# Kernel tuning notes

Hardware: AMD Instinct MI355X
Metric: run time of the kernel (lower is better)

The kernel has to match this reference:

```python
import jax, jax.numpy as jnp
import numpy as np

N, R, A, F, T, O = 50000, 5, 8, 128, 2, 128
RADIUS = 1.0

def _template_vertices():
    # polar grid of template vertices in cartesian coords, shape (R, A, 2)
    radii = (np.arange(1, R + 1) / R) * RADIUS
    angles = np.linspace(0.0, 2.0 * np.pi, A, endpoint=False)
    x = radii[:, None] * np.cos(angles)[None, :]
    y = radii[:, None] * np.sin(angles)[None, :]
    return np.stack([x, y], axis=-1)

def _interp_coeffs():
    # Gaussian interpolation coefficients (concrete define_interpolation_coefficients),
    # shape (R, A, R*A), rows normalized -- constant, non-trainable (built in build()).
    v = _template_vertices().reshape(R * A, 2)
    d2 = ((v[:, None, :] - v[None, :, :]) ** 2).sum(-1)
    sigma = RADIUS / R
    w = np.exp(-d2 / (2.0 * sigma ** 2))
    w = w / w.sum(axis=1, keepdims=True)
    return w.reshape(R, A, R * A).astype(np.float32)

def setup_inputs() -> dict:
    key = jax.random.key(0)
    k1, k2, k3, k4, k5 = jax.random.split(key, 5)
    mesh_signal = jax.random.normal(k1, (N, F), dtype=jnp.float32)
    bary_w = jax.random.uniform(k2, (N, R, A, 3), dtype=jnp.float32)
    bary_w = bary_w / bary_w.sum(axis=-1, keepdims=True)  # barycentric weights sum to 1
    bary_idx = jax.random.randint(k3, (N, R, A, 3), 0, N, dtype=jnp.int32)
    glorot = lambda k, shp: jax.random.uniform(
        k, shp, jnp.float32, -1.0, 1.0) * np.sqrt(6.0 / (shp[-1] + shp[-2]))
    template_weights = glorot(k4, (A, T, O, F))  # (n_angular, templates, out, feat)
    bias = glorot(k5, (T, O))
    return {"mesh_signal": mesh_signal, "bary_w": bary_w,
            "template_weights": template_weights, "bias": bias,
            "interp_coeffs": jnp.asarray(_interp_coeffs()),
            "bary_idx": bary_idx}

def reference(mesh_signal, bary_w, template_weights, bias, interp_coeffs, bary_idx):
    # --- patch operator: barycentric gather + interpolation ---
    gathered = mesh_signal[bary_idx]                       # (N,R,A,3,F) irregular gather
    interp = (bary_w[..., None] * gathered).sum(axis=-2)   # (N,R,A,F)
    # prior: mix all R*A template-vertex signals per output template vertex
    sig = interp.reshape(-1, R * A, F)                     # (N,RA,F)
    interp = jnp.einsum('nkf,rak->nraf', sig, interp_coeffs)  # (N,R,A,F)
    # --- fold: all A rotations (rotation_delta=1), vectorized by rolling weights ---
    rots = jnp.arange(0, A, 1)                             # K = A rotations
    idx = (jnp.arange(A)[None, :] + rots[:, None]) % A     # (K,A): roll(interp,+r) == roll(W,-r)
    W_all = template_weights[idx]                          # (K,A,T,O,F)
    # TF adds bias before summing over (R,A) axes -> bias appears R*A times
    z = jnp.einsum('nraf,katof->nkto', interp, W_all) + (R * A) * bias  # (N,K,T,O)
    out = jax.nn.relu(z).sum(axis=2)                       # sum over templates -> (N,K,O)
    return out
```

## Files before the change

### kernel.cpp

```cpp
#include <hip/hip_runtime.h>
#include <hip/hip_bf16.h>
#include <stdint.h>

#define NN 50000
#define RR 5
#define AA 8
#define FF 128
#define TT 2
#define OO 128
#define KDIM 1024
#define KB 512
#define RA 40

typedef __attribute__((ext_vector_type(8))) short short8;
typedef __attribute__((ext_vector_type(4))) float f32x4;
typedef __attribute__((ext_vector_type(4))) int i32x4;

__device__ inline void gload_lds16(const void* g, void* l) {
  __builtin_amdgcn_global_load_lds(
      (const __attribute__((address_space(1))) unsigned int*)g,
      (__attribute__((address_space(3))) unsigned int*)l, 16, 0, 0);
}

__global__ void prep_kernel(const float* __restrict__ mesh,
                            const float* __restrict__ coeffs,
                            const float* __restrict__ W,
                            const float* __restrict__ bary_w,
                            const int* __restrict__ bary_idx,
                            __hip_bfloat16* __restrict__ meshq,
                            float* __restrict__ G,
                            __hip_bfloat16* __restrict__ Bh,
                            unsigned* __restrict__ packb,
                            int do_pack) {
  int tid = blockIdx.x * blockDim.x + threadIdx.x;
  int stride = gridDim.x * blockDim.x;
  for (int i = tid; i < NN * FF; i += stride) {
    int n = i >> 7, f = i & 127;
    int p = f >> 5, fo = f & 31;
    meshq[((long)p * NN + n) * 32 + fo] = __float2bfloat16(mesh[i]);
  }
  for (int i = tid; i < AA * RA; i += stride) {
    int p = i / RA, k = i % RA;
    int a = p & 3;
    float s1 = 0.f, s2 = 0.f;
    for (int r = 0; r < RR; ++r) {
      s1 += coeffs[(r * AA + a) * RA + k];
      s2 += coeffs[(r * AA + a + 4) * RA + k];
    }
    G[i] = (p < 4) ? (s1 + s2) : (s1 - s2);
  }
  for (int i = tid; i < 2048 * KB; i += stride) {
    int col = i >> 9, k = i & 511;
    int half = col >> 10, c = col & 1023;
    int o = c >> 3, t = (c >> 2) & 1, j = c & 3;
    int a4 = k >> 7, f = k & 127;
    int m = (a4 + j) & 3;
    float w0 = W[((m * TT + t) * OO + o) * FF + f];
    float w4 = W[(((m + 4) * TT + t) * OO + o) * FF + f];
    float v;
    if (half == 0) v = 0.5f * (w0 + w4);
    else {
      v = 0.5f * (w0 - w4);
      if (a4 + j >= 4) v = -v;
    }
    Bh[i] = __float2bfloat16(v);
  }
  if (do_pack) {
    for (int i = tid; i < NN * 120; i += stride) {
      __hip_bfloat16 h = __float2bfloat16(bary_w[i]);
      unsigned wb = *(unsigned short*)&h;
      packb[i] = ((unsigned)bary_idx[i] << 16) | wb;
    }
  }
}

__global__ __launch_bounds__(256) void s_pass_packed(
    const __hip_bfloat16* __restrict__ meshq,
    const unsigned* __restrict__ packb,
    const float* __restrict__ G,
    __hip_bfloat16* __restrict__ Sout,
    int p) {
  __shared__ unsigned pk_s[16 * 120];
  __shared__ float g_s[AA * RA];
  int tid = threadIdx.x;
  long n0 = (long)blockIdx.x * 16;
  const i32x4* psrc = (const i32x4*)(packb + n0 * 120);
  for (int i = tid; i < 480; i += 256) {
    i32x4 v = __builtin_nontemporal_load(psrc + i);
    ((i32x4*)pk_s)[i] = v;
  }
  for (int i = tid; i < AA * RA; i += 256) g_s[i] = G[i];
  __syncthreads();

  int g = tid >> 4;
  int fo = tid & 15;
  long n = n0 + g;
  const unsigned* pg = pk_s + g * 120;
  const char* mbase = (const char*)meshq + (long)p * NN * 64 + fo * 4;

  float sx_acc[AA], sy_acc[AA];
#pragma unroll
  for (int a = 0; a < AA; ++a) { sx_acc[a] = 0.f; sy_acc[a] = 0.f; }

#pragma unroll 2
  for (int k = 0; k < RA; ++k) {
    float sx = 0.f, sy = 0.f;
#pragma unroll
    for (int j = 0; j < 3; ++j) {
      unsigned v = pg[k * 3 + j];
      unsigned row = v >> 16;
      float w = __uint_as_float(v << 16);
      unsigned u = *(const unsigned*)(mbase + (long)row * 64);
      sx += w * __uint_as_float(u << 16);
      sy += w * __uint_as_float(u & 0xffff0000u);
    }
#pragma unroll
    for (int a = 0; a < AA; ++a) {
      float c = g_s[a * RA + k];
      sx_acc[a] += c * sx;
      sy_acc[a] += c * sy;
    }
  }

  long base = n * KDIM + p * 32 + fo * 2;
#pragma unroll
  for (int a = 0; a < AA; ++a) {
    __hip_bfloat16 hx = __float2bfloat16(sx_acc[a]);
    __hip_bfloat16 hy = __float2bfloat16(sy_acc[a]);
    unsigned u = (unsigned)*(unsigned short*)&hx | ((unsigned)*(unsigned short*)&hy << 16);
    __builtin_nontemporal_store(u, (unsigned*)(Sout + base + a * FF));
  }
}

__global__ __launch_bounds__(256) void s_pass_kernel(
    const __hip_bfloat16* __restrict__ meshq,
    const float* __restrict__ bary_w,
    const int* __restrict__ bary_idx,
    const float* __restrict__ G,
    __hip_bfloat16* __restrict__ Sout,
    int p) {
  __shared__ float w_s[16 * 120];
  __shared__ int i_s[16 * 120];
  __shared__ float g_s[AA * RA];
  int tid = threadIdx.x;
  long n0 = (long)blockIdx.x * 16;
  const f32x4* wsrc = (const f32x4*)(bary_w + n0 * 120);
  const i32x4* isrc = (const i32x4*)(bary_idx + n0 * 120);
  for (int i = tid; i < 480; i += 256) {
    f32x4 wv = __builtin_nontemporal_load(wsrc + i);
    ((f32x4*)w_s)[i] = wv;
    i32x4 iv = __builtin_nontemporal_load(isrc + i);
    ((i32x4*)i_s)[i] = iv;
  }
  for (int i = tid; i < AA * RA; i += 256) g_s[i] = G[i];
  __syncthreads();
  int g = tid >> 4;
  int fo = tid & 15;
  long n = n0 + g;
  const float* wg = w_s + g * 120;
  const int* ig = i_s + g * 120;
  const char* mbase = (const char*)meshq + (long)p * NN * 64 + fo * 4;
  float sx_acc[AA], sy_acc[AA];
#pragma unroll
  for (int a = 0; a < AA; ++a) { sx_acc[a] = 0.f; sy_acc[a] = 0.f; }
#pragma unroll 2
  for (int k = 0; k < RA; ++k) {
    float sx = 0.f, sy = 0.f;
#pragma unroll
    for (int j = 0; j < 3; ++j) {
      int row = ig[k * 3 + j];
      unsigned u = *(const unsigned*)(mbase + (long)row * 64);
      float w = wg[k * 3 + j];
      sx += w * __uint_as_float(u << 16);
      sy += w * __uint_as_float(u & 0xffff0000u);
    }
#pragma unroll
    for (int a = 0; a < AA; ++a) {
      float c = g_s[a * RA + k];
      sx_acc[a] += c * sx;
      sy_acc[a] += c * sy;
    }
  }
  long base = n * KDIM + p * 32 + fo * 2;
#pragma unroll
  for (int a = 0; a < AA; ++a) {
    __hip_bfloat16 hx = __float2bfloat16(sx_acc[a]);
    __hip_bfloat16 hy = __float2bfloat16(sy_acc[a]);
    unsigned u = (unsigned)*(unsigned short*)&hx | ((unsigned)*(unsigned short*)&hy << 16);
    __builtin_nontemporal_store(u, (unsigned*)(Sout + base + a * FF));
  }
}

__global__ __launch_bounds__(256, 2) void gemm_kernel(
    const __hip_bfloat16* __restrict__ Sh,
    const __hip_bfloat16* __restrict__ Bh,
    const float* __restrict__ bias,
    float* __restrict__ out) {
  int bx = blockIdx.x;
  int by = blockIdx.y;
  int cb = by & 7;
  int mt = ((by >> 3) << 3) + bx;
  if (mt >= 391) return;
  int row0 = mt * 128;
  int cE0 = cb * 128;

  int tid = threadIdx.x;
  int lane = tid & 63;
  int wid = tid >> 6;
  int wave_m = wid >> 1;
  int wave_n = wid & 1;

  __shared__ __align__(16) char lds[79872];

  long srcSp[2], srcB[2];
  int dstA[2], dstBd[2];
#pragma unroll
  for (int i = 0; i < 2; ++i) {
    int li = i * 256 + tid;
    int r = li >> 2, sp = li & 3;
    int sl = sp ^ ((r >> 1) & 3);
    int rowA = row0 + r;
    if (rowA >= NN) rowA = NN - 1;
    srcSp[i] = (long)rowA * KDIM + sl * 8;
    dstA[i] = li * 16;
    srcB[i] = (long)(cE0 + r) * KB + sl * 8;
    dstBd[i] = 16384 + li * 16;
  }
  int offA[4], offB[4];
#pragma unroll
  for (int m = 0; m < 4; ++m) {
    int r = wave_m * 64 + m * 16 + (lane & 15);
    int phys = (lane >> 4) ^ ((r >> 1) & 3);
    offA[m] = r * 64 + phys * 16;
  }
#pragma unroll
  for (int n = 0; n < 4; ++n) {
    int c = wave_n * 64 + n * 16 + (lane & 15);
    int phys = (lane >> 4) ^ ((c >> 1) & 3);
    offB[n] = 16384 + c * 64 + phys * 16;
  }

  f32x4 acc[4][8];
#pragma unroll
  for (int m = 0; m < 4; ++m)
#pragma unroll
    for (int q = 0; q < 8; ++q) acc[m][q] = (f32x4){0.f, 0.f, 0.f, 0.f};

#define STAGE(T)                                                              \
  {                                                                           \
    char* base_ = lds + ((T) & 1) * 32768;                                    \
    long k0_ = (long)(T) * 32;                                                \
    _Pragma("unroll") for (int i_ = 0; i_ < 2; ++i_)                          \
        gload_lds16(Sh + srcSp[i_] + k0_, base_ + dstA[i_]);                  \
    _Pragma("unroll") for (int i_ = 0; i_ < 2; ++i_)                          \
        gload_lds16(Sh + srcSp[i_] + 512 + k0_, base_ + 8192 + dstA[i_]);     \
    _Pragma("unroll") for (int i_ = 0; i_ < 2; ++i_)                          \
        gload_lds16(Bh + srcB[i_] + k0_, base_ + dstBd[i_]);                  \
    _Pragma("unroll") for (int i_ = 0; i_ < 2; ++i_)                          \
        gload_lds16(Bh + srcB[i_] + (long)1024 * KB + k0_,                    \
                    base_ + 8192 + dstBd[i_]);                                \
  }

#define GSTEP(STP, DOSTAGE)                                                   \
  {                                                                           \
    const char* cbuf = lds + ((STP) & 1) * 32768;                             \
    asm volatile("s_waitcnt vmcnt(0)" ::: "memory");                          \
    __builtin_amdgcn_sched_barrier(0);                                        \
    __builtin_amdgcn_s_barrier();                                             \
    __builtin_amdgcn_sched_barrier(0);                                        \
    short8 aE[4], aO[4], bE[4], bO[4];                                        \
    _Pragma("unroll") for (int m_ = 0; m_ < 4; ++m_) {                        \
      aE[m_] = *(const short8*)(cbuf + offA[m_]);                             \
      aO[m_] = *(const short8*)(cbuf + offA[m_] + 8192);                      \
    }                                                                         \
    _Pragma("unroll") for (int n_ = 0; n_ < 4; ++n_) {                        \
      bE[n_] = *(const short8*)(cbuf + offB[n_]);                             \
      bO[n_] = *(const short8*)(cbuf + offB[n_] + 8192);                      \
    }                                                                         \
    if (DOSTAGE) STAGE((STP) + 1)                                             \
    __builtin_amdgcn_s_setprio(1);                                            \
    _Pragma("unroll") for (int m_ = 0; m_ < 4; ++m_)                          \
        _Pragma("unroll") for (int n_ = 0; n_ < 4; ++n_) {                    \
      acc[m_][n_] = __builtin_amdgcn_mfma_f32_16x16x32_bf16(                  \
          aE[m_], bE[n_], acc[m_][n_], 0, 0, 0);                              \
      acc[m_][n_ + 4] = __builtin_amdgcn_mfma_f32_16x16x32_bf16(              \
          aO[m_], bO[n_], acc[m_][n_ + 4], 0, 0, 0);                          \
    }                                                                         \
    __builtin_amdgcn_s_setprio(0);                                            \
    __builtin_amdgcn_sched_barrier(0);                                        \
  }

  STAGE(0)
  GSTEP(0, 1)  GSTEP(1, 1)  GSTEP(2, 1)  GSTEP(3, 1)
  GSTEP(4, 1)  GSTEP(5, 1)  GSTEP(6, 1)  GSTEP(7, 1)
  GSTEP(8, 1)  GSTEP(9, 1)  GSTEP(10, 1) GSTEP(11, 1)
  GSTEP(12, 1) GSTEP(13, 1) GSTEP(14, 1) GSTEP(15, 0)

  __syncthreads();
  float* lout = (float*)lds;
  int c = lane & 15;
  int t = (c >> 2) & 1;
  int j = c & 3;
  int hi = lane >> 4;
  float bq[4];
#pragma unroll
  for (int n = 0; n < 4; ++n) {
    int o_l = wave_n * 8 + n * 2 + (c >> 3);
    bq[n] = 40.f * bias[t * OO + cb * 16 + o_l];
  }
#pragma unroll
  for (int m = 0; m < 4; ++m) {
#pragma unroll
    for (int n = 0; n < 4; ++n) {
      int o_l = wave_n * 8 + n * 2 + (c >> 3);
#pragma unroll
      for (int i = 0; i < 4; ++i) {
        float zE = acc[m][n][i];
        float zO = acc[m][n + 4][i];
        float rlo = fmaxf(zE + zO + bq[n], 0.f);
        float rhi = fmaxf(zE - zO + bq[n], 0.f);
        rlo += __shfl_xor(rlo, 4);
        rhi += __shfl_xor(rhi, 4);
        if (!(lane & 4)) {
          int node = wave_m * 64 + m * 16 + hi * 4 + i;
          lout[node * 156 + j * 20 + o_l] = rlo;
          lout[node * 156 + (j + 4) * 20 + o_l] = rhi;
        }
      }
    }
  }
  __syncthreads();

#pragma unroll
  for (int it = 0; it < 16; ++it) {
    int gi = it * 256 + tid;
    int node = gi >> 5;
    int rem = gi & 31;
    int kr = rem >> 2, o4 = rem & 3;
    int grow = row0 + node;
    if (grow < NN) {
      f32x4 v = *(const f32x4*)(lout + node * 156 + kr * 20 + o4 * 4);
      long gaddr = (long)grow * 1024 + kr * 128 + cb * 16 + o4 * 4;
      __builtin_nontemporal_store(v, (f32x4*)(out + gaddr));
    }
  }
}

extern "C" void kernel_launch(void* const* d_in, const int* in_sizes, int n_in,
                              void* d_out, int out_size, void* d_ws, size_t ws_size,
                              hipStream_t stream) {
  const float* mesh   = (const float*)d_in[0];
  const float* bary_w = (const float*)d_in[1];
  const float* W      = (const float*)d_in[2];
  const float* bias   = (const float*)d_in[3];
  const float* coeffs = (const float*)d_in[4];
  const int* bidx     = (const int*)d_in[5];
  float* out = (float*)d_out;
  char* ws = (char*)d_ws;

  __hip_bfloat16* meshq = (__hip_bfloat16*)ws;
  float* G              = (float*)(ws + 12800000);
  __hip_bfloat16* Bh    = (__hip_bfloat16*)(ws + 12801280);
  __hip_bfloat16* Smat  = (__hip_bfloat16*)(ws + 16995584);
  unsigned* packb       = (unsigned*)(ws + 119395584);

  int do_pack = (ws_size >= 143395584UL) ? 1 : 0;

  prep_kernel<<<dim3(2048), dim3(256), 0, stream>>>(mesh, coeffs, W, bary_w, bidx,
                                                    meshq, G, Bh, packb, do_pack);
  if (do_pack) {
    for (int p = 0; p < 4; ++p)
      s_pass_packed<<<dim3(3125), dim3(256), 0, stream>>>(meshq, packb, G, Smat, p);
  } else {
    for (int p = 0; p < 4; ++p)
      s_pass_kernel<<<dim3(3125), dim3(256), 0, stream>>>(meshq, bary_w, bidx, G, Smat, p);
  }
  gemm_kernel<<<dim3(8, 392), dim3(256), 0, stream>>>(Smat, Bh, bias, out);
}
```

Before: 388.8 us.

## Widen gather per thread with packed FMA and issue GEMM prefetch earlier

The packed gather pass now handles 32 nodes per block with 8 threads per node. Each thread loads 8 bytes (4 bf16 features) per neighbor and accumulates them with packed f32x2 FMAs, halving the block count and doubling work per thread. This is meant to cut gather instruction count and per-block packb staging overhead, at the cost of fewer threads in flight to hide the random gather latency. Separately, the GEMM main loop now issues the next-stage global-to-LDS copies right after the barrier, before the LDS fragment reads, to start the memory traffic sooner.

New measurement: 375.6 us. 1.04x faster.

```diff
diff --git a/kernel.cpp b/kernel.cpp
--- a/kernel.cpp
+++ b/kernel.cpp
@@ -14,7 +14,21 @@
 
 typedef __attribute__((ext_vector_type(8))) short short8;
 typedef __attribute__((ext_vector_type(4))) float f32x4;
+typedef __attribute__((ext_vector_type(2))) float f32x2;
 typedef __attribute__((ext_vector_type(4))) int i32x4;
+typedef __attribute__((ext_vector_type(2))) unsigned u32x2;
+
+#if __has_builtin(__builtin_elementwise_fma)
+__device__ inline f32x2 pk_fma(f32x2 a, f32x2 b, f32x2 c) {
+  return __builtin_elementwise_fma(a, b, c);
+}
+#else
+__device__ inline f32x2 pk_fma(f32x2 a, f32x2 b, f32x2 c) {
+  f32x2 d;
+  asm("v_pk_fma_f32 %0, %1, %2, %3" : "=v"(d) : "v"(a), "v"(b), "v"(c));
+  return d;
+}
+#endif
 
 __device__ inline void gload_lds16(const void* g, void* l) {
   __builtin_amdgcn_global_load_lds(
@@ -80,55 +94,73 @@
     const float* __restrict__ G,
     __hip_bfloat16* __restrict__ Sout,
     int p) {
-  __shared__ unsigned pk_s[16 * 120];
+  __shared__ unsigned pk_s[32 * 120];
   __shared__ float g_s[AA * RA];
   int tid = threadIdx.x;
-  long n0 = (long)blockIdx.x * 16;
+  long n0 = (long)blockIdx.x * 32;
+  int nnode = (NN - n0 < 32) ? (int)(NN - n0) : 32;
+  int nvec = nnode * 30;
   const i32x4* psrc = (const i32x4*)(packb + n0 * 120);
-  for (int i = tid; i < 480; i += 256) {
+  for (int i = tid; i < nvec; i += 256) {
     i32x4 v = __builtin_nontemporal_load(psrc + i);
     ((i32x4*)pk_s)[i] = v;
   }
   for (int i = tid; i < AA * RA; i += 256) g_s[i] = G[i];
   __syncthreads();
 
-  int g = tid >> 4;
-  int fo = tid & 15;
+  int g = tid >> 3;
+  int fo = tid & 7;
   long n = n0 + g;
+  if (n >= NN) return;
   const unsigned* pg = pk_s + g * 120;
-  const char* mbase = (const char*)meshq + (long)p * NN * 64 + fo * 4;
-
-  float sx_acc[AA], sy_acc[AA];
-#pragma unroll
-  for (int a = 0; a < AA; ++a) { sx_acc[a] = 0.f; sy_acc[a] = 0.f; }
+  const char* mbase = (const char*)meshq + (long)p * NN * 64 + fo * 8;
+
+  f32x2 accA[AA], accB[AA];
+#pragma unroll
+  for (int a = 0; a < AA; ++a) {
+    accA[a] = (f32x2){0.f, 0.f};
+    accB[a] = (f32x2){0.f, 0.f};
+  }
 
 #pragma unroll 2
   for (int k = 0; k < RA; ++k) {
-    float sx = 0.f, sy = 0.f;
+    f32x2 sA = (f32x2){0.f, 0.f}, sB = (f32x2){0.f, 0.f};
 #pragma unroll
     for (int j = 0; j < 3; ++j) {
       unsigned v = pg[k * 3 + j];
-      unsigned row = v >> 16;
+      long row = v >> 16;
       float w = __uint_as_float(v << 16);
-      unsigned u = *(const unsigned*)(mbase + (long)row * 64);
-      sx += w * __uint_as_float(u << 16);
-      sy += w * __uint_as_float(u & 0xffff0000u);
+      f32x2 wv = (f32x2){w, w};
+      u32x2 u = *(const u32x2*)(mbase + row * 64);
+      f32x2 lo = (f32x2){__uint_as_float(u[0] << 16),
+                         __uint_as_float(u[0] & 0xffff0000u)};
+      f32x2 hi = (f32x2){__uint_as_float(u[1] << 16),
+                         __uint_as_float(u[1] & 0xffff0000u)};
+      sA = pk_fma(wv, lo, sA);
+      sB = pk_fma(wv, hi, sB);
     }
 #pragma unroll
     for (int a = 0; a < AA; ++a) {
-      float c = g_s[a * RA + k];
-      sx_acc[a] += c * sx;
-      sy_acc[a] += c * sy;
-    }
-  }
-
-  long base = n * KDIM + p * 32 + fo * 2;
+      float cc = g_s[a * RA + k];
+      f32x2 cv = (f32x2){cc, cc};
+      accA[a] = pk_fma(cv, sA, accA[a]);
+      accB[a] = pk_fma(cv, sB, accB[a]);
+    }
+  }
+
+  long base = n * KDIM + p * 32 + fo * 4;
 #pragma unroll
   for (int a = 0; a < AA; ++a) {
-    __hip_bfloat16 hx = __float2bfloat16(sx_acc[a]);
-    __hip_bfloat16 hy = __float2bfloat16(sy_acc[a]);
-    unsigned u = (unsigned)*(unsigned short*)&hx | ((unsigned)*(unsigned short*)&hy << 16);
-    __builtin_nontemporal_store(u, (unsigned*)(Sout + base + a * FF));
+    __hip_bfloat16 h0 = __float2bfloat16(accA[a][0]);
+    __hip_bfloat16 h1 = __float2bfloat16(accA[a][1]);
+    __hip_bfloat16 h2 = __float2bfloat16(accB[a][0]);
+    __hip_bfloat16 h3 = __float2bfloat16(accB[a][1]);
+    unsigned w0 = (unsigned)*(unsigned short*)&h0 |
+                  ((unsigned)*(unsigned short*)&h1 << 16);
+    unsigned w1 = (unsigned)*(unsigned short*)&h2 |
+                  ((unsigned)*(unsigned short*)&h3 << 16);
+    u32x2 st = (u32x2){w0, w1};
+    __builtin_nontemporal_store(st, (u32x2*)(Sout + base + a * FF));
   }
 }
 
@@ -268,6 +300,8 @@
     __builtin_amdgcn_sched_barrier(0);                                        \
     __builtin_amdgcn_s_barrier();                                             \
     __builtin_amdgcn_sched_barrier(0);                                        \
+    if (DOSTAGE) STAGE((STP) + 1)                                             \
+    __builtin_amdgcn_sched_barrier(0);                                        \
     short8 aE[4], aO[4], bE[4], bO[4];                                        \
     _Pragma("unroll") for (int m_ = 0; m_ < 4; ++m_) {                        \
       aE[m_] = *(const short8*)(cbuf + offA[m_]);                             \
@@ -277,7 +311,6 @@
       bE[n_] = *(const short8*)(cbuf + offB[n_]);                             \
       bO[n_] = *(const short8*)(cbuf + offB[n_] + 8192);                      \
     }                                                                         \
-    if (DOSTAGE) STAGE((STP) + 1)                                             \
     __builtin_amdgcn_s_setprio(1);                                            \
     _Pragma("unroll") for (int m_ = 0; m_ < 4; ++m_)                          \
         _Pragma("unroll") for (int n_ = 0; n_ < 4; ++n_) {                    \
@@ -370,7 +403,7 @@
                                                     meshq, G, Bh, packb, do_pack);
   if (do_pack) {
     for (int p = 0; p < 4; ++p)
-      s_pass_packed<<<dim3(3125), dim3(256), 0, stream>>>(meshq, packb, G, Smat, p);
+      s_pass_packed<<<dim3(1563), dim3(256), 0, stream>>>(meshq, packb, G, Smat, p);
   } else {
     for (int p = 0; p < 4; ++p)
       s_pass_kernel<<<dim3(3125), dim3(256), 0, stream>>>(meshq, bary_w, bidx, G, Smat, p);
```
